# Kernel tuning notes

Measured on AMD Instinct MI355X. Metric: run time of the kernel, lower is better.

The kernel has to match this reference:

```python
import jax, jax.numpy as jnp
import numpy as np

D_MODEL = 1024
N_HEADS = 16
HEAD_DIM = D_MODEL // N_HEADS  # 64
SEQ = 2048
BATCH = 2


def setup_inputs() -> dict:
    key = jax.random.key(0)
    ks = jax.random.split(key, 12)
    s = 1.0 / np.sqrt(D_MODEL)
    return {
        "query": jax.random.normal(ks[0], (SEQ, BATCH, D_MODEL), jnp.float32),
        "key": jax.random.normal(ks[1], (SEQ, BATCH, D_MODEL), jnp.float32),
        "value": jax.random.normal(ks[2], (SEQ, BATCH, D_MODEL), jnp.float32),
        "Wq": jax.random.normal(ks[3], (D_MODEL, D_MODEL), jnp.float32) * s,
        "bq": jax.random.normal(ks[4], (D_MODEL,), jnp.float32) * s,
        "Wk": jax.random.normal(ks[5], (D_MODEL, D_MODEL), jnp.float32) * s,
        "bk": jax.random.normal(ks[6], (D_MODEL,), jnp.float32) * s,
        "Wv": jax.random.normal(ks[7], (D_MODEL, D_MODEL), jnp.float32) * s,
        "bv": jax.random.normal(ks[8], (D_MODEL,), jnp.float32) * s,
        "Wo": jax.random.normal(ks[9], (D_MODEL, D_MODEL), jnp.float32) * s,
        "bo": jax.random.normal(ks[10], (D_MODEL,), jnp.float32) * s,
    }


def _rope_tables(seq_len):
    # theta_i = 1 / 10000^(2i/head_dim), i in [0, head_dim//2)
    theta = 1.0 / (10000.0 ** (2.0 * jnp.arange(HEAD_DIM // 2, dtype=jnp.float32) / HEAD_DIM))
    pos = jnp.arange(seq_len, dtype=jnp.float32)[:, None, None, None] * theta  # [S,1,1,hd/2]
    return jnp.sin(pos), jnp.cos(pos)


def _apply_rope(t, sin, cos):
    # t: [S, B, H, hd]; NOTE faithful to source: t2 = q1*sin - q2*cos (minus)
    h = HEAD_DIM // 2
    q1, q2 = t[..., :h], t[..., h:]
    return jnp.concatenate([q1 * cos - q2 * sin, q1 * sin - q2 * cos], axis=-1)


def reference(query, key, value, Wq, bq, Wk, bk, Wv, bv, Wo, bo):
    S, B, _ = query.shape
    q = (query @ Wq.T + bq).reshape(S, B, N_HEADS, HEAD_DIM)
    k = (key @ Wk.T + bk).reshape(S, B, N_HEADS, HEAD_DIM)
    v = (value @ Wv.T + bv).reshape(S, B, N_HEADS, HEAD_DIM)
    sin, cos = _rope_tables(S)
    q = _apply_rope(q, sin, cos)
    k = _apply_rope(k, sin, cos)
    # [S,B,H,d] -> [B,H,S,d]
    q = q.transpose(1, 2, 0, 3)
    k = k.transpose(1, 2, 0, 3)
    v = v.transpose(1, 2, 0, 3)
    scale = 1.0 / jnp.sqrt(jnp.float32(HEAD_DIM))
    scores = jnp.einsum("bhqd,bhkd->bhqk", q, k) * scale
    attn = jax.nn.softmax(scores, axis=-1)
    out = jnp.einsum("bhqk,bhkd->bhqd", attn, v)  # [B,H,S,d]
    out = out.transpose(2, 0, 1, 3).reshape(S, B, D_MODEL)
    return out @ Wo.T + bo
```

## Files before the change

### kernel.cpp

```cpp
#include <hip/hip_runtime.h>
#include <hip/hip_bf16.h>

#define DMODEL 1024
#define NHEADS 16
#define HDIM   64
#define SEQ    2048
#define BATCH  2
#define MROWS  (SEQ*BATCH)

typedef unsigned int u32;
typedef unsigned short u16;
typedef __attribute__((ext_vector_type(8))) short bfrag;
typedef __attribute__((ext_vector_type(4))) float f32x4;
typedef __attribute__((ext_vector_type(16))) float f32x16;
typedef union { u32 u[4]; bfrag f; } fragu;

#define LOG2E 1.44269504088896341f

__device__ __forceinline__ u32 f2bf(float x) {
    unsigned u = __float_as_uint(x);
    return (u + 0x7fffu + ((u >> 16) & 1u)) >> 16;
}
__device__ __forceinline__ float bf2f(u32 h) {
    return __uint_as_float(h << 16);
}
__device__ __forceinline__ u32 pk2bf(float a, float b) {
    __hip_bfloat162 t = __float22bfloat162_rn(make_float2(a, b));
    u32 r;
    __builtin_memcpy(&r, &t, 4);
    return r;
}
__device__ __forceinline__ float fexp2(float x) {
#if __has_builtin(__builtin_amdgcn_exp2f)
    return __builtin_amdgcn_exp2f(x);
#else
    return exp2f(x);
#endif
}

__device__ __forceinline__ void gld16(const void* g, void* l) {
    __builtin_amdgcn_global_load_lds(
        (const __attribute__((address_space(1))) unsigned int*)g,
        (__attribute__((address_space(3))) unsigned int*)l, 16, 0, 0);
}


__global__ __launch_bounds__(256) void prep_kernel(
    const float* __restrict__ Wq, const float* __restrict__ Wk,
    const float* __restrict__ Wv, const float* __restrict__ Wo,
    float* __restrict__ query, float* __restrict__ key, float* __restrict__ value,
    u16* __restrict__ wqb, u16* __restrict__ wkb, u16* __restrict__ wvb,
    u16* __restrict__ wob, float2* __restrict__ tab)
{
    const int y = blockIdx.y;
    if (y == 3) {
        if (blockIdx.x >= 256) return;
        const int e = blockIdx.x * 256 + threadIdx.x;
        const int s = e >> 5, i = e & 31;
        const double th = exp(-(double)i * (9.210340371976184 / 32.0));
        double sn, cs;
        sincos((double)s * th, &sn, &cs);
        tab[e] = make_float2((float)sn, (float)cs);
        return;
    }
    if (y < 3 || y == 7) {
        const float* src = (y == 0) ? Wq : (y == 1) ? Wk : (y == 2) ? Wv : Wo;
        u16* dst = (y == 0) ? wqb : (y == 1) ? wkb : (y == 2) ? wvb : wob;
        const int i = blockIdx.x * 256 + threadIdx.x;
        const int e0  = i * 8;
        const int row = e0 >> 10, k = e0 & 1023, t = k >> 5, j0 = k & 31;
        float xs[8];
        *(float4*)&xs[0] = ((const float4*)src)[i * 2];
        *(float4*)&xs[4] = ((const float4*)src)[i * 2 + 1];
        __align__(16) u16 hb[8];
        __align__(16) u16 lb[8];
        #pragma unroll
        for (int j = 0; j < 8; ++j) {
            const u32 h = f2bf(xs[j]);
            hb[j] = (u16)h;
            lb[j] = (u16)f2bf(xs[j] - bf2f(h));
        }
        u16* o = dst + (size_t)row * 2048 + t * 64 + j0;
        *(uint4*)o        = *(const uint4*)hb;
        *(uint4*)(o + 32) = *(const uint4*)lb;
        return;
    }
    float* io = (y == 4) ? query : (y == 5) ? key : value;
    const int gi = blockIdx.x * 256 + threadIdx.x;
    uint4* io4 = (uint4*)io + (size_t)gi * 8;
    uint4 raw[8];
    #pragma unroll
    for (int j = 0; j < 8; ++j) raw[j] = io4[j];
    __align__(16) u16 hb[32];
    __align__(16) u16 lb[32];
    #pragma unroll
    for (int j = 0; j < 32; ++j) {
        const float x = __uint_as_float(((const u32*)raw)[j]);
        const u32 h = f2bf(x);
        hb[j] = (u16)h;
        lb[j] = (u16)f2bf(x - bf2f(h));
    }
    #pragma unroll
    for (int j = 0; j < 4; ++j) io4[j]     = ((const uint4*)hb)[j];
    #pragma unroll
    for (int j = 0; j < 4; ++j) io4[4 + j] = ((const uint4*)lb)[j];
}

template <int NI>
__device__ __forceinline__ void gemm_body(
    int id, int mode,
    const u16* __restrict__ Ab, const u16* __restrict__ Wb,
    const float* __restrict__ bias, const float2* __restrict__ tab,
    float rope_scale,
    u16* __restrict__ Oh, u16* __restrict__ Ol, float* __restrict__ Of,
    u16* smem16)
{
    u16* sA = smem16;
    u16* sB = smem16 + 16384;

    const int tid   = threadIdx.x;
    const int w     = tid >> 6;
    const int lane  = tid & 63;
    const int lrow  = lane & 15;
    const int lquad = lane >> 4;

    const int NBLK = 1024 / (NI * 16);
    const int xcd  = id & 7;
    const int jj   = id >> 3;
    const int nblk = jj & (NBLK - 1);
    const int mblk = (xcd << 2) | (jj / NBLK);
    const int n0   = nblk * NI * 16;
    const int m0   = mblk * 128;

    const int srow8 = lane >> 3;
    const int sch   = (lane & 7) ^ srow8;

    int aoffh[2], aoffl[2], boffh[NI], boffl[NI];
    #pragma unroll
    for (int mi = 0; mi < 2; ++mi) {
        const int ra = w * 32 + mi * 16 + lrow;
        aoffh[mi] = ra * 64 + ((lquad ^ (ra & 7)) << 3);
        aoffl[mi] = ra * 64 + (((lquad + 4) ^ (ra & 7)) << 3);
    }
    #pragma unroll
    for (int ni = 0; ni < NI; ++ni) {
        const int rb = ni * 16 + lrow;
        boffh[ni] = rb * 64 + ((lquad ^ (rb & 7)) << 3);
        boffl[ni] = rb * 64 + (((lquad + 4) ^ (rb & 7)) << 3);
    }

    f32x4 acc[2][NI] = {};

    auto stage = [&](int t) {
        const int h = t & 1;
        #pragma unroll
        for (int i = 0; i < 4; ++i) {
            const int slab = w * 4 + i;
            const int row  = slab * 8 + srow8;
            gld16(Ab + (size_t)(m0 + row) * 2048 + t * 64 + sch * 8,
                  sA + h * 8192 + slab * 512);
        }
        #pragma unroll
        for (int i = 0; i < NI / 2; ++i) {
            const int slab = w * (NI / 2) + i;
            const int row  = slab * 8 + srow8;
            gld16(Wb + (size_t)(n0 + row) * 2048 + t * 64 + sch * 8,
                  sB + h * (NI * 1024) + slab * 512);
        }
    };

    stage(0);
    for (int t = 0; t < 32; ++t) {
        __syncthreads();
        if (t < 31) stage(t + 1);
        const int h = t & 1;
        const u16* sAh_ = sA + h * 8192;
        const u16* sBh_ = sB + h * (NI * 1024);

        bfrag ah[2], al[2], bh[NI], bl[NI];
        #pragma unroll
        for (int mi = 0; mi < 2; ++mi) {
            ah[mi] = *(const bfrag*)&sAh_[aoffh[mi]];
            al[mi] = *(const bfrag*)&sAh_[aoffl[mi]];
        }
        #pragma unroll
        for (int ni = 0; ni < NI; ++ni) {
            bh[ni] = *(const bfrag*)&sBh_[boffh[ni]];
            bl[ni] = *(const bfrag*)&sBh_[boffl[ni]];
        }

        #pragma unroll
        for (int mi = 0; mi < 2; ++mi)
            #pragma unroll
            for (int ni = 0; ni < NI; ++ni) {
                acc[mi][ni] = __builtin_amdgcn_mfma_f32_16x16x32_bf16(ah[mi], bh[ni], acc[mi][ni], 0, 0, 0);
                acc[mi][ni] = __builtin_amdgcn_mfma_f32_16x16x32_bf16(ah[mi], bl[ni], acc[mi][ni], 0, 0, 0);
                acc[mi][ni] = __builtin_amdgcn_mfma_f32_16x16x32_bf16(al[mi], bh[ni], acc[mi][ni], 0, 0, 0);
            }
    }

    float bn[NI];
    #pragma unroll
    for (int ni = 0; ni < NI; ++ni) bn[ni] = bias[n0 + ni * 16 + lrow];

    if constexpr (NI == 4) {
        if (mode == 0) {
            const int hblk = nblk;
            #pragma unroll
            for (int mi = 0; mi < 2; ++mi)
                #pragma unroll
                for (int r = 0; r < 4; ++r) {
                    const int mrow = w * 32 + mi * 16 + lquad * 4 + r;
                    const int m  = m0 + mrow;
                    const int bb = m & 1;
                    const int sg = m >> 1;
                    const size_t ob = (((size_t)(bb * NHEADS + hblk) * SEQ) + sg) * HDIM;
                    #pragma unroll
                    for (int ni = 0; ni < 2; ++ni) {
                        const int i = ni * 16 + lrow;
                        const float2 sc = tab[(size_t)sg * 32 + i];
                        const float x1 = acc[mi][ni][r]     + bn[ni];
                        const float x2 = acc[mi][ni + 2][r] + bn[ni + 2];
                        const float o1 = (x1 * sc.y - x2 * sc.x) * rope_scale;
                        const float o2 = (x1 * sc.x - x2 * sc.y) * rope_scale;
                        const u32 h1 = f2bf(o1);
                        const u32 h2 = f2bf(o2);
                        Oh[ob + i]      = (u16)h1;  Ol[ob + i]      = (u16)f2bf(o1 - bf2f(h1));
                        Oh[ob + i + 32] = (u16)h2;  Ol[ob + i + 32] = (u16)f2bf(o2 - bf2f(h2));
                    }
                }
            return;
        }
        if (mode == 1) {
            __syncthreads();
            u32* vb = (u32*)smem16;
            #pragma unroll
            for (int mi = 0; mi < 2; ++mi)
                #pragma unroll
                for (int r = 0; r < 4; ++r) {
                    const int mrow = w * 32 + mi * 16 + lquad * 4 + r;
                    const int bb = mrow & 1;
                    const int sl = mrow >> 1;
                    #pragma unroll
                    for (int ni = 0; ni < 4; ++ni) {
                        const int d = ni * 16 + lrow;
                        vb[bb * 4160 + d * 65 + sl] = f2bf(acc[mi][ni][r] + bn[ni]);
                    }
                }
            __syncthreads();
            const int hblk = nblk;
            #pragma unroll
            for (int rep = 0; rep < 4; ++rep) {
                const int c  = rep * 256 + tid;
                const int bb = c >> 9;
                const int d  = (c >> 3) & 63;
                const int s8 = c & 7;
                __align__(8) u16 hb[8];
                #pragma unroll
                for (int j = 0; j < 8; ++j)
                    hb[j] = (u16)vb[bb * 4160 + d * 65 + s8 * 8 + j];
                const size_t orow = ((size_t)(bb * NHEADS + hblk) * HDIM + d) * SEQ + (m0 >> 1);
                const int blk16 = (s8 >> 1) * 16;
                const int off   = (s8 & 1) * 4;
                *(uint2*)&Oh[orow + blk16 + off]     = *(const uint2*)&hb[0];
                *(uint2*)&Oh[orow + blk16 + 8 + off] = *(const uint2*)&hb[4];
            }
            return;
        }
    }
    #pragma unroll
    for (int mi = 0; mi < 2; ++mi)
        #pragma unroll
        for (int r = 0; r < 4; ++r) {
            const int m = m0 + w * 32 + mi * 16 + lquad * 4 + r;
            #pragma unroll
            for (int ni = 0; ni < NI; ++ni)
                Of[(size_t)m * 1024 + n0 + ni * 16 + lrow] = acc[mi][ni][r] + bn[ni];
        }
}

__global__ __launch_bounds__(256) void qkv_gemm_kernel(
    const u16* __restrict__ query, const u16* __restrict__ key,
    const u16* __restrict__ value,
    const u16* __restrict__ Wqb, const u16* __restrict__ Wkb,
    const u16* __restrict__ Wvb,
    const float* __restrict__ bq, const float* __restrict__ bk,
    const float* __restrict__ bv, const float2* __restrict__ tab,
    u16* __restrict__ Qh, u16* __restrict__ Ql,
    u16* __restrict__ Kh, u16* __restrict__ Kl,
    u16* __restrict__ VTh)
{
    __shared__ u16 smem16[24576];
    const int z  = blockIdx.z;
    const int id = blockIdx.x + 16 * blockIdx.y;
    const u16* A    = (z == 0) ? query : (z == 1) ? key : value;
    const u16* Wb   = (z == 0) ? Wqb : (z == 1) ? Wkb : Wvb;
    const float* bb = (z == 0) ? bq : (z == 1) ? bk : bv;
    u16* Oh = (z == 0) ? Qh : (z == 1) ? Kh : VTh;
    u16* Ol = (z == 0) ? Ql : (z == 1) ? Kl : nullptr;
    const int mode = (z == 2) ? 1 : 0;
    const float scale = (z == 0) ? 0.125f * LOG2E : 1.0f;
    gemm_body<4>(id, mode, A, Wb, bb, tab, scale, Oh, Ol, nullptr, smem16);
}

__global__ __launch_bounds__(256) void out_gemm_kernel(
    const u16* __restrict__ Ab, const u16* __restrict__ Wb,
    const float* __restrict__ bias, float* __restrict__ Of)
{
    __shared__ u16 smem16[20480];
    const int id = blockIdx.x + 32 * blockIdx.y;
    gemm_body<2>(id, 2, Ab, Wb, bias, nullptr, 1.0f, nullptr, nullptr, Of, smem16);
}

__global__ __launch_bounds__(256) void attn_mfma_kernel(
    const u16* __restrict__ Qh, const u16* __restrict__ Ql,
    const u16* __restrict__ Kh, const u16* __restrict__ Kl,
    const u16* __restrict__ Vh,
    u16* __restrict__ AOb)
{
    __shared__ u16 sKh[8192], sKl[8192];
    __shared__ u16 sVh[8192];

    const int tid  = threadIdx.x;
    const int w    = tid >> 6;
    const int lane = tid & 63;
    const int l31  = lane & 31;
    const int g    = lane >> 5;

    const int id = blockIdx.x + 16 * blockIdx.y;
    const int jj = id >> 3;
    const int bh = ((id & 7) << 2) | (jj >> 4);
    const int qt = jj & 15;

    const size_t qg = ((size_t)bh * SEQ + qt * 128 + w * 32 + l31) * HDIM + g * 8;
    bfrag qfh[4], qfl[4];
    #pragma unroll
    for (int ks = 0; ks < 4; ++ks) {
        qfh[ks] = *(const bfrag*)&Qh[qg + ks * 16];
        qfl[ks] = *(const bfrag*)&Ql[qg + ks * 16];
    }

    const int srow   = lane >> 3;
    const int schunk = (lane & 7) ^ srow;
    const u16* gsrc = nullptr; u16* lbase = nullptr; size_t istep = 0, ktstep = 0;
    if (w == 0) {
        gsrc = Kh + ((size_t)bh * SEQ + srow) * HDIM + schunk * 8;
        istep = 8 * 64; ktstep = 64 * 64; lbase = sKh;
    } else if (w == 1) {
        gsrc = Kl + ((size_t)bh * SEQ + srow) * HDIM + schunk * 8;
        istep = 8 * 64; ktstep = 64 * 64; lbase = sKl;
    } else if (w == 2) {
        gsrc = Vh + ((size_t)bh * HDIM + srow) * SEQ + schunk * 8;
        istep = 8 * SEQ; ktstep = 64; lbase = sVh;
    }

    int koff[2][4];
    #pragma unroll
    for (int a = 0; a < 2; ++a) {
        const int row = a * 32 + l31;
        #pragma unroll
        for (int c = 0; c < 4; ++c)
            koff[a][c] = row * 64 + (((c * 2 + g) ^ (row & 7)) << 3);
    }

    f32x16 accO[2] = {};
    float l_loc = 0.0f;

    auto stage = [&](int kt) {
        if (w < 3) {
            const u16* gp = gsrc + (size_t)kt * ktstep;
            u16* dst = lbase + (kt & 1) * 4096;
            #pragma unroll
            for (int i = 0; i < 8; ++i)
                gld16(gp + (size_t)i * istep, dst + i * 512);
        }
    };

    stage(0);
    for (int kt = 0; kt < SEQ / 64; ++kt) {
        __syncthreads();
        if (kt < SEQ / 64 - 1) stage(kt + 1);
        const int po = (kt & 1) * 4096;

        f32x16 accS[2] = {};
        #pragma unroll
        for (int kg = 0; kg < 2; ++kg)
            #pragma unroll
            for (int ks = 0; ks < 4; ++ks) {
                const bfrag kh_ = *(const bfrag*)&sKh[po + koff[kg][ks]];
                const bfrag kl_ = *(const bfrag*)&sKl[po + koff[kg][ks]];
                accS[kg] = __builtin_amdgcn_mfma_f32_32x32x16_bf16(kh_, qfh[ks], accS[kg], 0, 0, 0);
                accS[kg] = __builtin_amdgcn_mfma_f32_32x32x16_bf16(kh_, qfl[ks], accS[kg], 0, 0, 0);
                accS[kg] = __builtin_amdgcn_mfma_f32_32x32x16_bf16(kl_, qfh[ks], accS[kg], 0, 0, 0);
            }

        float pv[2][16];
        #pragma unroll
        for (int kg = 0; kg < 2; ++kg)
            #pragma unroll
            for (int r = 0; r < 16; ++r) {
                const float p = fexp2(accS[kg][r]);
                pv[kg][r] = p;
                l_loc += p;
            }

        #pragma unroll
        for (int kp = 0; kp < 4; ++kp) {
            const int kg = kp >> 1;
            const int t8 = (kp & 1) * 8;
            fragu ph;
            #pragma unroll
            for (int j2 = 0; j2 < 4; ++j2)
                ph.u[j2] = pk2bf(pv[kg][t8 + 2 * j2], pv[kg][t8 + 2 * j2 + 1]);
            #pragma unroll
            for (int dt = 0; dt < 2; ++dt) {
                const bfrag vh = *(const bfrag*)&sVh[po + koff[dt][kp]];
                accO[dt] = __builtin_amdgcn_mfma_f32_32x32x16_bf16(vh, ph.f, accO[dt], 0, 0, 0);
            }
        }
    }

    const float inv = 1.0f / (l_loc + __shfl_xor(l_loc, 32));

    const int b = bh >> 4;
    const int h = bh & 15;
    const int sg = qt * 128 + w * 32 + l31;
    const int rm = sg * BATCH + b;
    #pragma unroll
    for (int dt = 0; dt < 2; ++dt)
        #pragma unroll
        for (int rq = 0; rq < 4; ++rq) {
            const int j0 = 8 * rq + 4 * g;
            const int t  = h * 2 + dt;
            __align__(8) u16 hb[4];
            __align__(8) u16 lb[4];
            #pragma unroll
            for (int i2 = 0; i2 < 4; ++i2) {
                const float v = accO[dt][rq * 4 + i2] * inv;
                const u32 hh = f2bf(v);
                hb[i2] = (u16)hh;
                lb[i2] = (u16)f2bf(v - bf2f(hh));
            }
            u16* o = AOb + (size_t)rm * 2048 + t * 64 + j0;
            *(uint2*)o        = *(const uint2*)hb;
            *(uint2*)(o + 32) = *(const uint2*)lb;
        }
}

extern "C" void kernel_launch(void* const* d_in, const int* in_sizes, int n_in,
                              void* d_out, int out_size, void* d_ws, size_t ws_size,
                              hipStream_t stream)
{
    float* query = (float*)d_in[0];
    float* key   = (float*)d_in[1];
    float* value = (float*)d_in[2];
    const float* Wq    = (const float*)d_in[3];
    const float* bq    = (const float*)d_in[4];
    const float* Wk    = (const float*)d_in[5];
    const float* bk    = (const float*)d_in[6];
    const float* Wv    = (const float*)d_in[7];
    const float* bv    = (const float*)d_in[8];
    const float* Wo    = (const float*)d_in[9];
    const float* bo    = (const float*)d_in[10];
    float* out = (float*)d_out;

    char* wsb = (char*)d_ws;
    const size_t MB = 1024 * 1024;
    u16* Wqb = (u16*)(wsb + 0 * MB);
    u16* Wkb = (u16*)(wsb + 4 * MB);
    u16* Wvb = (u16*)(wsb + 8 * MB);
    float2* tab = (float2*)(wsb + 12 * MB);
    u16* Qh  = (u16*)(wsb + 16 * MB); u16* Ql  = (u16*)(wsb + 24 * MB);
    u16* Kh  = (u16*)(wsb + 32 * MB); u16* Kl  = (u16*)(wsb + 40 * MB);
    u16* VTh = (u16*)(wsb + 48 * MB);
    u16* Wob = (u16*)(wsb + 56 * MB);
    u16* AOb = (u16*)(wsb + 0 * MB);

    prep_kernel<<<dim3(512, 8), 256, 0, stream>>>(
        Wq, Wk, Wv, Wo, query, key, value, Wqb, Wkb, Wvb, Wob, tab);
    qkv_gemm_kernel<<<dim3(16, 32, 3), 256, 0, stream>>>(
        (const u16*)query, (const u16*)key, (const u16*)value,
        Wqb, Wkb, Wvb, bq, bk, bv, tab, Qh, Ql, Kh, Kl, VTh);
    attn_mfma_kernel<<<dim3(16, 32), 256, 0, stream>>>(
        Qh, Ql, Kh, Kl, VTh, AOb);
    out_gemm_kernel<<<dim3(32, 32), 256, 0, stream>>>(AOb, Wob, bo, out);
}
```

Measured before the change: 321.8 us.

## Split attention KV range in two and merge partials in a combine kernel

The attention kernel now runs a z-dimension of two, each block covering half of the key tiles. Each half writes unnormalised fp32 partial outputs and row sums, using the output buffer as scratch for the second half. A new combine kernel adds the two halves, normalises them and emits the hi/lo bf16 split that the output GEMM expects. Separately, the prep kernel's fp32-to-bf16 split loop is rewritten so each wave handles contiguous float4 chunks, for better coalescing. The aim is more blocks in flight for attention, at the cost of an extra launch and extra fp32 traffic for the partials.

Result: no change. 327.6 us (+1.8%).

```diff
diff --git a/kernel.cpp b/kernel.cpp
--- a/kernel.cpp
+++ b/kernel.cpp
@@ -63,47 +63,39 @@
         tab[e] = make_float2((float)sn, (float)cs);
         return;
     }
+    const float* src;
+    u16* dst;
+    int nr;
     if (y < 3 || y == 7) {
-        const float* src = (y == 0) ? Wq : (y == 1) ? Wk : (y == 2) ? Wv : Wo;
-        u16* dst = (y == 0) ? wqb : (y == 1) ? wkb : (y == 2) ? wvb : wob;
-        const int i = blockIdx.x * 256 + threadIdx.x;
-        const int e0  = i * 8;
-        const int row = e0 >> 10, k = e0 & 1023, t = k >> 5, j0 = k & 31;
-        float xs[8];
-        *(float4*)&xs[0] = ((const float4*)src)[i * 2];
-        *(float4*)&xs[4] = ((const float4*)src)[i * 2 + 1];
-        __align__(16) u16 hb[8];
-        __align__(16) u16 lb[8];
-        #pragma unroll
-        for (int j = 0; j < 8; ++j) {
-            const u32 h = f2bf(xs[j]);
-            hb[j] = (u16)h;
-            lb[j] = (u16)f2bf(xs[j] - bf2f(h));
-        }
-        u16* o = dst + (size_t)row * 2048 + t * 64 + j0;
-        *(uint4*)o        = *(const uint4*)hb;
-        *(uint4*)(o + 32) = *(const uint4*)lb;
-        return;
-    }
-    float* io = (y == 4) ? query : (y == 5) ? key : value;
-    const int gi = blockIdx.x * 256 + threadIdx.x;
-    uint4* io4 = (uint4*)io + (size_t)gi * 8;
-    uint4 raw[8];
-    #pragma unroll
-    for (int j = 0; j < 8; ++j) raw[j] = io4[j];
-    __align__(16) u16 hb[32];
-    __align__(16) u16 lb[32];
-    #pragma unroll
-    for (int j = 0; j < 32; ++j) {
-        const float x = __uint_as_float(((const u32*)raw)[j]);
-        const u32 h = f2bf(x);
-        hb[j] = (u16)h;
-        lb[j] = (u16)f2bf(x - bf2f(h));
-    }
-    #pragma unroll
-    for (int j = 0; j < 4; ++j) io4[j]     = ((const uint4*)hb)[j];
-    #pragma unroll
-    for (int j = 0; j < 4; ++j) io4[4 + j] = ((const uint4*)lb)[j];
+        src = (y == 0) ? Wq : (y == 1) ? Wk : (y == 2) ? Wv : Wo;
+        dst = (y == 0) ? wqb : (y == 1) ? wkb : (y == 2) ? wvb : wob;
+        nr = 2;
+    } else {
+        float* io = (y == 4) ? query : (y == 5) ? key : value;
+        src = io;
+        dst = (u16*)io;
+        nr = 8;
+    }
+    const int lane = threadIdx.x & 63;
+    const int wv   = threadIdx.x >> 6;
+    const int g8   = lane >> 3;
+    const int l8   = lane & 7;
+    for (int r = 0; r < nr; ++r) {
+        const size_t kb = (size_t)blockIdx.x * (4 * nr) + (size_t)r * 4 + wv;
+        const float4 x4 = *(const float4*)(src + kb * 256 + lane * 4);
+        __align__(8) u16 hb[4];
+        __align__(8) u16 lb[4];
+        const float xs[4] = {x4.x, x4.y, x4.z, x4.w};
+        #pragma unroll
+        for (int i = 0; i < 4; ++i) {
+            const u32 h = f2bf(xs[i]);
+            hb[i] = (u16)h;
+            lb[i] = (u16)f2bf(xs[i] - bf2f(h));
+        }
+        u16* o = dst + kb * 512 + g8 * 64 + l8 * 4;
+        *(uint2*)o        = *(const uint2*)hb;
+        *(uint2*)(o + 32) = *(const uint2*)lb;
+    }
 }
 
 template <int NI>
@@ -316,7 +308,7 @@
     const u16* __restrict__ Qh, const u16* __restrict__ Ql,
     const u16* __restrict__ Kh, const u16* __restrict__ Kl,
     const u16* __restrict__ Vh,
-    u16* __restrict__ AOb)
+    float* __restrict__ O0, float* __restrict__ O1, float* __restrict__ lsum)
 {
     __shared__ u16 sKh[8192], sKl[8192];
     __shared__ u16 sVh[8192];
@@ -326,6 +318,7 @@
     const int lane = tid & 63;
     const int l31  = lane & 31;
     const int g    = lane >> 5;
+    const int z    = blockIdx.z;
 
     const int id = blockIdx.x + 16 * blockIdx.y;
     const int jj = id >> 3;
@@ -376,10 +369,11 @@
         }
     };
 
-    stage(0);
-    for (int kt = 0; kt < SEQ / 64; ++kt) {
+    const int kt0 = z * 16;
+    stage(kt0);
+    for (int kt = kt0; kt < kt0 + 16; ++kt) {
         __syncthreads();
-        if (kt < SEQ / 64 - 1) stage(kt + 1);
+        if (kt < kt0 + 15) stage(kt + 1);
         const int po = (kt & 1) * 4096;
 
         f32x16 accS[2] = {};
@@ -420,31 +414,63 @@
         }
     }
 
-    const float inv = 1.0f / (l_loc + __shfl_xor(l_loc, 32));
+    const float ls = l_loc + __shfl_xor(l_loc, 32);
 
     const int b = bh >> 4;
     const int h = bh & 15;
     const int sg = qt * 128 + w * 32 + l31;
     const int rm = sg * BATCH + b;
+    if (lane < 32)
+        lsum[(size_t)z * 65536 + (size_t)bh * 2048 + sg] = ls;
+    float* Op = z ? O1 : O0;
     #pragma unroll
     for (int dt = 0; dt < 2; ++dt)
         #pragma unroll
         for (int rq = 0; rq < 4; ++rq) {
-            const int j0 = 8 * rq + 4 * g;
-            const int t  = h * 2 + dt;
-            __align__(8) u16 hb[4];
-            __align__(8) u16 lb[4];
-            #pragma unroll
-            for (int i2 = 0; i2 < 4; ++i2) {
-                const float v = accO[dt][rq * 4 + i2] * inv;
-                const u32 hh = f2bf(v);
-                hb[i2] = (u16)hh;
-                lb[i2] = (u16)f2bf(v - bf2f(hh));
-            }
-            u16* o = AOb + (size_t)rm * 2048 + t * 64 + j0;
-            *(uint2*)o        = *(const uint2*)hb;
-            *(uint2*)(o + 32) = *(const uint2*)lb;
-        }
+            float4 v4;
+            v4.x = accO[dt][rq * 4 + 0];
+            v4.y = accO[dt][rq * 4 + 1];
+            v4.z = accO[dt][rq * 4 + 2];
+            v4.w = accO[dt][rq * 4 + 3];
+            *(float4*)&Op[(size_t)rm * 1024 + (h * 2 + dt) * 32 + 8 * rq + 4 * g] = v4;
+        }
+}
+
+__global__ __launch_bounds__(256) void combine_kernel(
+    float* __restrict__ O0, const float* __restrict__ O1,
+    const float* __restrict__ lsum)
+{
+    const int lane = threadIdx.x & 63;
+    const int wv   = threadIdx.x >> 6;
+    const int g8   = lane >> 3;
+    const int l8   = lane & 7;
+    #pragma unroll
+    for (int r = 0; r < 8; ++r) {
+        const size_t kb = (size_t)blockIdx.x * 32 + (size_t)r * 4 + wv;
+        const int rm = (int)(kb >> 2);
+        const int t  = ((int)kb & 3) * 8 + g8;
+        const int b  = rm & 1;
+        const int sg = rm >> 1;
+        const int h  = t >> 1;
+        const float l0 = lsum[(size_t)(b * 16 + h) * 2048 + sg];
+        const float l1 = lsum[65536 + (size_t)(b * 16 + h) * 2048 + sg];
+        const float inv = 1.0f / (l0 + l1);
+        const float4 x0 = *(const float4*)(O0 + kb * 256 + lane * 4);
+        const float4 x1 = *(const float4*)(O1 + kb * 256 + lane * 4);
+        const float xs[4] = {x0.x + x1.x, x0.y + x1.y, x0.z + x1.z, x0.w + x1.w};
+        __align__(8) u16 hb[4];
+        __align__(8) u16 lb[4];
+        #pragma unroll
+        for (int i = 0; i < 4; ++i) {
+            const float v = xs[i] * inv;
+            const u32 hh = f2bf(v);
+            hb[i] = (u16)hh;
+            lb[i] = (u16)f2bf(v - bf2f(hh));
+        }
+        u16* o = (u16*)O0 + kb * 512 + g8 * 64 + l8 * 4;
+        *(uint2*)o        = *(const uint2*)hb;
+        *(uint2*)(o + 32) = *(const uint2*)lb;
+    }
 }
 
 extern "C" void kernel_launch(void* const* d_in, const int* in_sizes, int n_in,
@@ -474,14 +500,17 @@
     u16* Kh  = (u16*)(wsb + 32 * MB); u16* Kl  = (u16*)(wsb + 40 * MB);
     u16* VTh = (u16*)(wsb + 48 * MB);
     u16* Wob = (u16*)(wsb + 56 * MB);
-    u16* AOb = (u16*)(wsb + 0 * MB);
+    float* O0   = (float*)(wsb + 0 * MB);
+    float* O1   = out;
+    float* lsum = (float*)(wsb + 60 * MB);
 
     prep_kernel<<<dim3(512, 8), 256, 0, stream>>>(
         Wq, Wk, Wv, Wo, query, key, value, Wqb, Wkb, Wvb, Wob, tab);
     qkv_gemm_kernel<<<dim3(16, 32, 3), 256, 0, stream>>>(
         (const u16*)query, (const u16*)key, (const u16*)value,
         Wqb, Wkb, Wvb, bq, bk, bv, tab, Qh, Ql, Kh, Kl, VTh);
-    attn_mfma_kernel<<<dim3(16, 32), 256, 0, stream>>>(
-        Qh, Ql, Kh, Kl, VTh, AOb);
-    out_gemm_kernel<<<dim3(32, 32), 256, 0, stream>>>(AOb, Wob, bo, out);
-}
+    attn_mfma_kernel<<<dim3(16, 32, 2), 256, 0, stream>>>(
+        Qh, Ql, Kh, Kl, VTh, O0, O1, lsum);
+    combine_kernel<<<dim3(512), 256, 0, stream>>>(O0, O1, lsum);
+    out_gemm_kernel<<<dim3(32, 32), 256, 0, stream>>>((const u16*)O0, Wob, bo, out);
+}
```
